# Optimization experiments

Hardware: AMD Instinct MI355X
Metric: run time of the kernel (lower is better)

Reference implementation:

```python
import jax, jax.numpy as jnp
import numpy as np

B = 2          # graphs (images)
GRID = 13      # patches per spatial dim -> N = 169 patches per image
N = GRID * GRID
NN = B * N     # total nodes
C = 256        # hidden_dim / out_channels per head
H = 4          # attention heads
L = 3          # GAT layers
LRELU_SLOPE = 0.2
LN_EPS = 1e-5


def _dense_edges():
    # fully-connected directed graph (i != j) per image, as in create_graph
    idx = np.arange(N)
    src, dst = np.meshgrid(idx, idx, indexing='ij')
    mask = src != dst
    src, dst = src[mask], dst[mask]              # [N*(N-1)]
    offs = (np.arange(B) * N)[:, None]
    e_src = (src[None, :] + offs).reshape(-1)
    e_dst = (dst[None, :] + offs).reshape(-1)
    return e_src.astype(np.int32), e_dst.astype(np.int32)


def setup_inputs() -> dict:
    key = jax.random.key(0)
    ks = jax.random.split(key, 8)
    s = 0.05
    e_src, e_dst = _dense_edges()
    return {
        'x':   jax.random.normal(ks[0], (NN, C), jnp.float32),
        'Wl':  jax.random.normal(ks[1], (L, C, H * C), jnp.float32) * s,
        'bl':  jnp.zeros((L, H * C), jnp.float32),
        'Wr':  jax.random.normal(ks[2], (L, C, H * C), jnp.float32) * s,
        'br':  jnp.zeros((L, H * C), jnp.float32),
        'att': jax.random.normal(ks[3], (L, H, C), jnp.float32) * s,
        'bias': jnp.zeros((L, C), jnp.float32),
        'ln_g': jnp.ones((L, C), jnp.float32),
        'ln_b': jnp.zeros((L, C), jnp.float32),
        'W1':  jax.random.normal(ks[4], (L, C, 2 * C), jnp.float32) * s,
        'b1':  jnp.zeros((L, 2 * C), jnp.float32),
        'W2':  jax.random.normal(ks[5], (L, 2 * C, C), jnp.float32) * s,
        'b2':  jnp.zeros((L, C), jnp.float32),
        'edge_src': jnp.asarray(e_src),
        'edge_dst': jnp.asarray(e_dst),
        'batch_ids': jnp.repeat(jnp.arange(B, dtype=jnp.int32), N),
    }


def _gatv2(x, Wl, bl, Wr, br, att, bias, src, dst, n_nodes):
    # PyG GATv2Conv, concat=False (mean over heads)
    xl = (x @ Wl + bl).reshape(n_nodes, H, C)   # source transform
    xr = (x @ Wr + br).reshape(n_nodes, H, C)   # target transform
    e = jax.nn.leaky_relu(xl[src] + xr[dst], LRELU_SLOPE)     # [E,H,C]
    logits = jnp.einsum('ehc,hc->eh', e, att)                 # [E,H]
    m = jax.ops.segment_max(logits, dst, num_segments=n_nodes)
    a = jnp.exp(logits - m[dst])
    z = jax.ops.segment_sum(a, dst, num_segments=n_nodes)
    alpha = a / (z[dst] + 1e-16)                              # softmax per target
    msg = alpha[:, :, None] * xl[src]                         # [E,H,C]
    agg = jax.ops.segment_sum(msg, dst, num_segments=n_nodes) # [N,H,C]
    return agg.mean(axis=1) + bias


def _layernorm(x, g, b):
    mu = x.mean(-1, keepdims=True)
    var = jnp.mean((x - mu) ** 2, -1, keepdims=True)
    return (x - mu) * jax.lax.rsqrt(var + LN_EPS) * g + b


def reference(x, Wl, bl, Wr, br, att, bias, ln_g, ln_b, W1, b1, W2, b2,
              edge_src, edge_dst, batch_ids):
    n_nodes = x.shape[0]
    for l in range(L):
        residual = x
        h = _gatv2(x, Wl[l], bl[l], Wr[l], br[l], att[l], bias[l],
                   edge_src, edge_dst, n_nodes)
        h = _layernorm(h, ln_g[l], ln_b[l])
        mlp = jnp.maximum(h @ W1[l] + b1[l], 0.0) @ W2[l] + b2[l]
        x = residual + mlp
    # global mean pool per graph
    sums = jax.ops.segment_sum(x, batch_ids, num_segments=B)
    cnts = jax.ops.segment_sum(jnp.ones((n_nodes, 1), x.dtype), batch_ids,
                               num_segments=B)
    return sums / cnts
```

## Files before the change

### kernel.cpp

```cpp
#include <hip/hip_runtime.h>
#include <hip/hip_bf16.h>

typedef __hip_bfloat16 bf16;
typedef __attribute__((ext_vector_type(8))) short short8v;
typedef __attribute__((ext_vector_type(4))) float float4v;

#define NNODES 169
#define NNTOT  338
#define CH     256
#define NH     4
#define NL     3
#define SPAD   176
#define TPAD   177
#define M1PAD  536
#define LN_EPS 1e-5f

__device__ __forceinline__ float b2f(bf16 v) { return __bfloat162float(v); }
__device__ __forceinline__ float lrelu(float v) { return fmaxf(v, 0.2f * v); }
__device__ __forceinline__ float ldm(const void* p, size_t i, int isbf) {
    return isbf ? b2f(((const bf16*)p)[i]) : ((const float*)p)[i];
}
__device__ __forceinline__ short f2bf(float f) {
    union { float f; unsigned u; } x; x.f = f;
    return (short)((x.u + 0x7FFFu + ((x.u >> 16) & 1u)) >> 16);
}
__device__ __forceinline__ int sniff_bf(const void* lng) {
    return ((((const unsigned*)lng)[0] & 0xFFFFu) == 0x3F80u) ? 1 : 0;
}

__global__ __launch_bounds__(256) void k_wt(
    const void* __restrict__ Wl, const void* __restrict__ Wr,
    const void* __restrict__ W1, const void* __restrict__ W2,
    short* __restrict__ wlT, short* __restrict__ wrT,
    short* __restrict__ w1T, short* __restrict__ w2T,
    const void* __restrict__ lng)
{
    __shared__ float s_t[32][33];
    const int isbf = sniff_bf(lng);
    const int z = blockIdx.z, mat = z & 3, l = z >> 2;
    const void* src; short* dst; int K, N;
    if      (mat == 0) { src = Wl; dst = wlT; K = CH;     N = NH * CH; }
    else if (mat == 1) { src = Wr; dst = wrT; K = CH;     N = NH * CH; }
    else if (mat == 2) { src = W1; dst = w1T; K = CH;     N = 2 * CH;  }
    else               { src = W2; dst = w2T; K = 2 * CH; N = CH;      }
    const int tiles = (K >> 5) * (N >> 5);
    if ((int)blockIdx.x >= tiles) return;
    const int tn = blockIdx.x % (N >> 5), tk = blockIdx.x / (N >> 5);
    const int k0 = tk * 32, n0 = tn * 32;
    const size_t lKN = (size_t)l * K * N;
    const int tx = threadIdx.x & 31, ty = threadIdx.x >> 5;

    for (int r = ty; r < 32; r += 8)
        s_t[r][tx] = ldm(src, lKN + (size_t)(k0 + r) * N + n0 + tx, isbf);
    __syncthreads();
    for (int r = ty; r < 32; r += 8)
        dst[lKN + (size_t)(n0 + r) * K + k0 + tx] = f2bf(s_t[tx][r]);
}

template<int KK, int ACT, int RES>
__device__ __forceinline__ void mfma_gemm(
    short* __restrict__ sA, short* __restrict__ sBT,
    const void* __restrict__ Av, int a_bf,
    const short* __restrict__ WT,
    const void* __restrict__ bv_, size_t oB, int isbf,
    const void* __restrict__ x_res, int r_bf,
    float* __restrict__ out,
    int M, int N, int row0, int col0)
{
    const int STR = KK + 8;
    const int tid = threadIdx.x, lane = tid & 63, w = tid >> 6;
    const int r = tid >> 2, q = tid & 3;
    const int kseg = KK / 4, kb0 = q * kseg;
    const int m = lane & 15, kb = (lane >> 4) * 8;
    const int w16 = w * 16;

    {
        const int gr = row0 + r;
        const int ok = (gr < M);
        if (a_bf) {
            const bf16* ap = (const bf16*)Av + (size_t)gr * KK + kb0;
            #pragma unroll
            for (int j = 0; j < kseg; j += 8) {
                int4 v = ok ? *(const int4*)(ap + j) : make_int4(0, 0, 0, 0);
                *(int4*)&sA[r * STR + kb0 + j] = v;
            }
        } else {
            const float* ap = (const float*)Av + (size_t)gr * KK + kb0;
            #pragma unroll
            for (int j = 0; j < kseg; j += 8) {
                short v8[8];
                if (ok) {
                    const float4 f0 = *(const float4*)(ap + j);
                    const float4 f1 = *(const float4*)(ap + j + 4);
                    v8[0] = f2bf(f0.x); v8[1] = f2bf(f0.y);
                    v8[2] = f2bf(f0.z); v8[3] = f2bf(f0.w);
                    v8[4] = f2bf(f1.x); v8[5] = f2bf(f1.y);
                    v8[6] = f2bf(f1.z); v8[7] = f2bf(f1.w);
                } else {
                    #pragma unroll
                    for (int u = 0; u < 8; u++) v8[u] = 0;
                }
                *(int4*)&sA[r * STR + kb0 + j] = *(int4*)v8;
            }
        }
        const short* bp = WT + (size_t)(col0 + r) * KK + kb0;
        #pragma unroll
        for (int j = 0; j < kseg; j += 8)
            *(int4*)&sBT[r * STR + kb0 + j] = *(const int4*)(bp + j);
    }
    __syncthreads();

    float4v acc[4];
    #pragma unroll
    for (int t = 0; t < 4; t++) acc[t] = (float4v){0.f, 0.f, 0.f, 0.f};

    #pragma unroll
    for (int kc = 0; kc < KK / 32; kc++) {
        const short8v af = *(const short8v*)&sA[(w16 + m) * STR + kc * 32 + kb];
        #pragma unroll
        for (int t = 0; t < 4; t++) {
            const short8v bfv = *(const short8v*)&sBT[(t * 16 + m) * STR + kc * 32 + kb];
            acc[t] = __builtin_amdgcn_mfma_f32_16x16x32_bf16(af, bfv, acc[t], 0, 0, 0);
        }
    }

    const int rq = (lane >> 4) * 4;
    #pragma unroll
    for (int t = 0; t < 4; t++) {
        const int col = col0 + t * 16 + m;
        const float bias_v = ldm(bv_, oB + col, isbf);
        #pragma unroll
        for (int rr = 0; rr < 4; rr++) {
            const int gr = row0 + w16 + rq + rr;
            if (gr >= M) continue;
            float v = acc[t][rr] + bias_v;
            if (ACT) v = fmaxf(v, 0.f);
            if (RES) v += ldm(x_res, (size_t)gr * N + col, r_bf);
            out[(size_t)gr * N + col] = v;
        }
    }
}

__global__ __launch_bounds__(256) void k_gemm_lr(
    const void* __restrict__ Av, int israw,
    const short* __restrict__ wlT, const short* __restrict__ wrT, size_t oWT,
    const void* __restrict__ bl, const void* __restrict__ br, size_t oB,
    float* __restrict__ xl, float* __restrict__ xr,
    const void* __restrict__ lng)
{
    __shared__ short sA[64 * 264];
    __shared__ short sBT[64 * 264];
    const int isbf = sniff_bf(lng);
    const int a_bf = israw ? isbf : 0;
    const int row0 = blockIdx.x * 64, col0 = blockIdx.y * 64;
    if (blockIdx.z == 0)
        mfma_gemm<256,0,0>(sA, sBT, Av, a_bf, wlT + oWT, bl, oB, isbf,
                           nullptr, 0, xl, NNTOT, NH * CH, row0, col0);
    else
        mfma_gemm<256,0,0>(sA, sBT, Av, a_bf, wrT + oWT, br, oB, isbf,
                           nullptr, 0, xr, NNTOT, NH * CH, row0, col0);
}

__global__ __launch_bounds__(256) void k_logits_sm(
    const float* __restrict__ xl, const float* __restrict__ xr,
    const void* __restrict__ att, size_t oA,
    float* __restrict__ alphaR, const void* __restrict__ lng)
{
    __shared__ float s_att[CH];
    __shared__ float s_xr[4 * CH];
    __shared__ float s_tile[64 * TPAD];
    __shared__ float s_log[4 * SPAD];
    const int isbf = sniff_bf(lng);
    const int g = blockIdx.z, h = blockIdx.y, d0 = blockIdx.x * 4;
    const int tid = threadIdx.x, lane = tid & 63, wv = tid >> 6;

    s_att[tid] = ldm(att, oA + h * CH + tid, isbf);
    #pragma unroll
    for (int i = 0; i < 4; i++) {
        const int d = d0 + i;
        s_xr[i * CH + tid] = (d < NNODES)
            ? xr[(size_t)(g * NNODES + d) * (NH * CH) + h * CH + tid] : 0.f;
    }

    float l0 = 0.f, l1 = 0.f, l2 = 0.f, l3 = 0.f;
    const int s = tid;
    for (int ch = 0; ch < 4; ch++) {
        __syncthreads();
        for (int i = tid; i < SPAD * 16; i += 256) {
            const int si = i >> 4, c4 = (i & 15) * 4;
            const float4 v = (si < NNODES)
                ? *(const float4*)(xl + (size_t)(g * NNODES + si) * (NH * CH)
                                   + h * CH + ch * 64 + c4)
                : make_float4(0.f, 0.f, 0.f, 0.f);
            s_tile[(c4 + 0) * TPAD + si] = v.x;
            s_tile[(c4 + 1) * TPAD + si] = v.y;
            s_tile[(c4 + 2) * TPAD + si] = v.z;
            s_tile[(c4 + 3) * TPAD + si] = v.w;
        }
        __syncthreads();
        if (s < NNODES) {
            const int cb = ch * 64;
            #pragma unroll 8
            for (int c = 0; c < 64; c++) {
                const float v = s_tile[c * TPAD + s];
                const float a = s_att[cb + c];
                l0 += a * lrelu(v + s_xr[cb + c]);
                l1 += a * lrelu(v + s_xr[CH + cb + c]);
                l2 += a * lrelu(v + s_xr[2 * CH + cb + c]);
                l3 += a * lrelu(v + s_xr[3 * CH + cb + c]);
            }
        }
    }
    if (s < NNODES) {
        s_log[s] = l0; s_log[SPAD + s] = l1;
        s_log[2 * SPAD + s] = l2; s_log[3 * SPAD + s] = l3;
    }
    __syncthreads();

    {
        const int d = d0 + wv;
        const float* row = s_log + wv * SPAD;
        const int s0 = lane, s1 = lane + 64, s2 = lane + 128;
        const float v0 = (s0 < NNODES && s0 != d) ? row[s0] : -1e30f;
        const float v1 = (s1 < NNODES && s1 != d) ? row[s1] : -1e30f;
        const float v2 = (s2 < NNODES && s2 != d) ? row[s2] : -1e30f;
        float mx = fmaxf(v0, fmaxf(v1, v2));
        mx = fmaxf(mx, __shfl_xor(mx, 32)); mx = fmaxf(mx, __shfl_xor(mx, 16));
        mx = fmaxf(mx, __shfl_xor(mx, 8));  mx = fmaxf(mx, __shfl_xor(mx, 4));
        mx = fmaxf(mx, __shfl_xor(mx, 2));  mx = fmaxf(mx, __shfl_xor(mx, 1));
        const float e0 = expf(v0 - mx), e1 = expf(v1 - mx), e2 = expf(v2 - mx);
        float z = e0 + e1 + e2;
        z += __shfl_xor(z, 32); z += __shfl_xor(z, 16); z += __shfl_xor(z, 8);
        z += __shfl_xor(z, 4);  z += __shfl_xor(z, 2);  z += __shfl_xor(z, 1);
        const float sc = 0.25f / (z + 1e-16f);
        if (d < NNODES) {
            float* arow = alphaR + ((size_t)(g * NH + h) * NNODES + d) * SPAD;
            if (s0 < NNODES) arow[s0] = e0 * sc;
            if (s1 < NNODES) arow[s1] = e1 * sc;
            if (s2 < NNODES) arow[s2] = e2 * sc;
        }
    }
}

__global__ __launch_bounds__(256) void k_agg(
    const float* __restrict__ alphaR, const float* __restrict__ xl,
    float* __restrict__ part)
{
    __shared__ float s_a[32 * 33];
    __shared__ float s_x[32 * 64];
    const int gh = blockIdx.z, g = gh >> 2, h = gh & 3;
    const int d0 = blockIdx.x * 32, c0 = blockIdx.y * 64;
    const int tid = threadIdx.x;
    const int dr = (tid >> 4) * 2, cq = (tid & 15) * 4;
    const int sr = tid >> 3, sc4 = (tid & 7) * 4;
    const int xc8 = (tid & 7) * 8;

    float acc[2][4] = {{0.f,0.f,0.f,0.f},{0.f,0.f,0.f,0.f}};

    for (int s0 = 0; s0 < NNODES; s0 += 32) {
        __syncthreads();
        {
            const int d = d0 + sr;
            const float* ap = alphaR + ((size_t)gh * NNODES + d) * SPAD + s0 + sc4;
            const int ok = (d < NNODES);
            s_a[sr * 33 + sc4 + 0] = (ok && s0 + sc4 + 0 < NNODES) ? ap[0] : 0.f;
            s_a[sr * 33 + sc4 + 1] = (ok && s0 + sc4 + 1 < NNODES) ? ap[1] : 0.f;
            s_a[sr * 33 + sc4 + 2] = (ok && s0 + sc4 + 2 < NNODES) ? ap[2] : 0.f;
            s_a[sr * 33 + sc4 + 3] = (ok && s0 + sc4 + 3 < NNODES) ? ap[3] : 0.f;
        }
        {
            const int sg = s0 + sr;
            if (sg < NNODES) {
                const float* xp = xl + (size_t)(g * NNODES + sg) * (NH * CH) + h * CH + c0 + xc8;
                *(float4*)&s_x[sr * 64 + xc8]     = *(const float4*)(xp);
                *(float4*)&s_x[sr * 64 + xc8 + 4] = *(const float4*)(xp + 4);
            } else {
                #pragma unroll
                for (int j = 0; j < 8; j++) s_x[sr * 64 + xc8 + j] = 0.f;
            }
        }
        __syncthreads();
        #pragma unroll
        for (int k = 0; k < 32; k++) {
            const float a0 = s_a[(dr + 0) * 33 + k];
            const float a1 = s_a[(dr + 1) * 33 + k];
            const float4 xv = *(const float4*)&s_x[k * 64 + cq];
            acc[0][0] += a0 * xv.x; acc[0][1] += a0 * xv.y;
            acc[0][2] += a0 * xv.z; acc[0][3] += a0 * xv.w;
            acc[1][0] += a1 * xv.x; acc[1][1] += a1 * xv.y;
            acc[1][2] += a1 * xv.z; acc[1][3] += a1 * xv.w;
        }
    }
    #pragma unroll
    for (int i = 0; i < 2; i++) {
        const int d = d0 + dr + i;
        if (d >= NNODES) continue;
        float4 v;
        v.x = acc[i][0]; v.y = acc[i][1]; v.z = acc[i][2]; v.w = acc[i][3];
        *(float4*)(part + ((size_t)h * NNTOT + g * NNODES + d) * CH + c0 + cq) = v;
    }
}

__global__ __launch_bounds__(256) void k_ln(
    const float* __restrict__ part,
    const void* __restrict__ bias, size_t oB,
    const void* __restrict__ ln_g, size_t oG,
    const void* __restrict__ ln_b, size_t oBt,
    float* __restrict__ h_out, const void* __restrict__ lng)
{
    __shared__ float s_red[8];
    const int isbf = sniff_bf(lng);
    const int node = blockIdx.x, c = threadIdx.x;
    const int lane = c & 63, wv = c >> 6;

    float vch = part[((size_t)0 * NNTOT + node) * CH + c]
              + part[((size_t)1 * NNTOT + node) * CH + c]
              + part[((size_t)2 * NNTOT + node) * CH + c]
              + part[((size_t)3 * NNTOT + node) * CH + c]
              + ldm(bias, oB + c, isbf);

    float s1 = vch, s2 = vch * vch;
    s1 += __shfl_xor(s1, 32); s2 += __shfl_xor(s2, 32);
    s1 += __shfl_xor(s1, 16); s2 += __shfl_xor(s2, 16);
    s1 += __shfl_xor(s1, 8);  s2 += __shfl_xor(s2, 8);
    s1 += __shfl_xor(s1, 4);  s2 += __shfl_xor(s2, 4);
    s1 += __shfl_xor(s1, 2);  s2 += __shfl_xor(s2, 2);
    s1 += __shfl_xor(s1, 1);  s2 += __shfl_xor(s2, 1);
    if (lane == 0) { s_red[wv] = s1; s_red[4 + wv] = s2; }
    __syncthreads();
    const float S1 = s_red[0] + s_red[1] + s_red[2] + s_red[3];
    const float S2 = s_red[4] + s_red[5] + s_red[6] + s_red[7];
    const float mu  = S1 * (1.f / CH);
    const float var = S2 * (1.f / CH) - mu * mu;
    const float o = (vch - mu) * rsqrtf(var + LN_EPS) * ldm(ln_g, oG + c, isbf)
                  + ldm(ln_b, oBt + c, isbf);
    h_out[(size_t)node * CH + c] = o;
}

__global__ __launch_bounds__(256) void k_mlp(
    const float* __restrict__ h_ln,
    const short* __restrict__ w1T, size_t oW1T,
    const void* __restrict__ b1, size_t oB1,
    const short* __restrict__ w2T, size_t oW2T,
    const void* __restrict__ b2, size_t oB2,
    const void* __restrict__ x_res, int israw,
    float* __restrict__ out, const void* __restrict__ lng)
{
    __shared__ short sA[16 * 264];
    __shared__ short sM1[16 * M1PAD];
    __shared__ short sW[64 * 520];
    const int isbf = sniff_bf(lng);
    const int r_bf = israw ? isbf : 0;
    const int g = blockIdx.y;
    const int d0 = blockIdx.x * 16;
    const int tid = threadIdx.x, lane = tid & 63, w = tid >> 6;
    const int m = lane & 15, kb = (lane >> 4) * 8, rq = (lane >> 4) * 4;
    const int w16 = w * 16;

    for (int i = tid; i < 16 * 64; i += 256) {
        const int si = i >> 6, c4 = (i & 63) * 4;
        const int d = d0 + si;
        const float4 v = (d < NNODES)
            ? *(const float4*)(h_ln + (size_t)(g * NNODES + d) * CH + c4)
            : make_float4(0.f, 0.f, 0.f, 0.f);
        short v4[4] = { f2bf(v.x), f2bf(v.y), f2bf(v.z), f2bf(v.w) };
        *(int2*)&sA[si * 264 + c4] = *(int2*)v4;
    }

    for (int nc = 0; nc < 8; nc++) {
        __syncthreads();
        for (int i = tid; i < 64 * 32; i += 256) {
            const int r = i >> 5, k8 = (i & 31) * 8;
            *(int4*)&sW[r * 264 + k8] =
                *(const int4*)(w1T + oW1T + (size_t)(nc * 64 + r) * 256 + k8);
        }
        __syncthreads();
        float4v acc = {0.f, 0.f, 0.f, 0.f};
        #pragma unroll
        for (int kc = 0; kc < 8; kc++) {
            const short8v af = *(const short8v*)&sA[m * 264 + kc * 32 + kb];
            const short8v bfv = *(const short8v*)&sW[(w16 + m) * 264 + kc * 32 + kb];
            acc = __builtin_amdgcn_mfma_f32_16x16x32_bf16(af, bfv, acc, 0, 0, 0);
        }
        const int ng = nc * 64 + w16 + m;
        const float bv = ldm(b1, oB1 + ng, isbf);
        #pragma unroll
        for (int rr = 0; rr < 4; rr++)
            sM1[(rq + rr) * M1PAD + ng] = f2bf(fmaxf(acc[rr] + bv, 0.f));
    }

    for (int nc = 0; nc < 4; nc++) {
        __syncthreads();
        for (int i = tid; i < 64 * 64; i += 256) {
            const int r = i >> 6, k8 = (i & 63) * 8;
            *(int4*)&sW[r * 520 + k8] =
                *(const int4*)(w2T + oW2T + (size_t)(nc * 64 + r) * 512 + k8);
        }
        __syncthreads();
        float4v acc = {0.f, 0.f, 0.f, 0.f};
        #pragma unroll
        for (int kc = 0; kc < 16; kc++) {
            const short8v af = *(const short8v*)&sM1[m * M1PAD + kc * 32 + kb];
            const short8v bfv = *(const short8v*)&sW[(w16 + m) * 520 + kc * 32 + kb];
            acc = __builtin_amdgcn_mfma_f32_16x16x32_bf16(af, bfv, acc, 0, 0, 0);
        }
        const int ng = nc * 64 + w16 + m;
        const float bv = ldm(b2, oB2 + ng, isbf);
        #pragma unroll
        for (int rr = 0; rr < 4; rr++) {
            const int d = d0 + rq + rr;
            if (d < NNODES) {
                const size_t ro = (size_t)(g * NNODES + d) * CH + ng;
                out[ro] = acc[rr] + bv + ldm(x_res, ro, r_bf);
            }
        }
    }
}

__global__ __launch_bounds__(256) void k_pool(const float* __restrict__ x,
                                              void* __restrict__ out,
                                              const void* __restrict__ lng) {
    const int isbf = sniff_bf(lng);
    const int g = blockIdx.x, c = threadIdx.x;
    float s = 0.f;
    const float* p = x + (size_t)g * NNODES * CH + c;
    #pragma unroll 8
    for (int n = 0; n < NNODES; n++) s += p[(size_t)n * CH];
    const float v = s * (1.f / NNODES);
    if (isbf) ((bf16*)out)[g * CH + c] = __float2bfloat16(v);
    else      ((float*)out)[g * CH + c] = v;
}

extern "C" void kernel_launch(void* const* d_in, const int* in_sizes, int n_in,
                              void* d_out, int out_size, void* d_ws, size_t ws_size,
                              hipStream_t stream)
{
    const void* x_in = d_in[0];
    const void* Wl   = d_in[1];
    const void* bl   = d_in[2];
    const void* Wr   = d_in[3];
    const void* br   = d_in[4];
    const void* att  = d_in[5];
    const void* bias = d_in[6];
    const void* lng  = d_in[7];
    const void* lnb  = d_in[8];
    const void* W1   = d_in[9];
    const void* b1   = d_in[10];
    const void* W2   = d_in[11];
    const void* b2   = d_in[12];

    float* ws     = (float*)d_ws;
    float* xl     = ws;
    float* xr     = xl + (size_t)NNTOT * NH * CH;
    float* alphaR = xr + (size_t)NNTOT * NH * CH;
    float* part   = alphaR + (size_t)2 * NH * NNODES * SPAD;
    float* h_ln   = part + (size_t)NH * NNTOT * CH;
    float* xa     = h_ln + (size_t)NNTOT * CH;
    float* xb     = xa + (size_t)NNTOT * CH;
    short* wlT    = (short*)(xb + (size_t)NNTOT * CH);
    short* wrT    = wlT + (size_t)NL * CH * NH * CH;
    short* w1T    = wrT + (size_t)NL * CH * NH * CH;
    short* w2T    = w1T + (size_t)NL * CH * 2 * CH;

    const size_t sB  = NH * CH;
    const size_t sA  = NH * CH;
    const size_t sC  = CH;
    const size_t sB1 = 2 * CH;
    const size_t sWT  = (size_t)CH * NH * CH;
    const size_t sW1T = (size_t)CH * 2 * CH;
    const size_t sW2T = (size_t)2 * CH * CH;

    k_wt<<<dim3(256, 1, 12), 256, 0, stream>>>(
        Wl, Wr, W1, W2, wlT, wrT, w1T, w2T, lng);

    const void* x_l[3] = { x_in, xa, xb };
    float*      x_o[3] = { xa, xb, xa };

    for (int l = 0; l < NL; l++) {
        const int israw = (l == 0);
        k_gemm_lr<<<dim3(6, 16, 2), 256, 0, stream>>>(
            x_l[l], israw, wlT, wrT, (size_t)l * sWT,
            bl, br, (size_t)l * sB, xl, xr, lng);
        k_logits_sm<<<dim3(43, NH, 2), 256, 0, stream>>>(
            xl, xr, att, (size_t)l * sA, alphaR, lng);
        k_agg<<<dim3(6, 4, 8), 256, 0, stream>>>(alphaR, xl, part);
        k_ln<<<dim3(NNTOT), 256, 0, stream>>>(
            part, bias, (size_t)l * sC, lng, (size_t)l * sC, lnb, (size_t)l * sC,
            h_ln, lng);
        k_mlp<<<dim3(11, 2), 256, 0, stream>>>(
            h_ln, w1T, (size_t)l * sW1T, b1, (size_t)l * sB1,
            w2T, (size_t)l * sW2T, b2, (size_t)l * sC,
            x_l[l], israw, x_o[l], lng);
    }

    k_pool<<<dim3(2), 256, 0, stream>>>(xa, d_out, lng);
}
```

Measured before the change: 395.2 us.

## Fuse LayerNorm into MLP first GEMM, split MLP into tiled kernels, widen logits block

LayerNorm is folded into a new kernel that also runs the first MLP GEMM over 64x64 output tiles on a 6x8 grid. The second MLP GEMM moves to the shared mfma_gemm helper on a 6x4 grid. The old MLP kernel ran on only 22 blocks, so this targets low parallelism and the h_ln round trip. In exchange, each first-GEMM block recomputes LayerNorm for its rows, and the intermediate m1 goes to global memory in fp32. The logits kernel now handles 8 destinations per block instead of 4, halving its grid, which reuses each xl tile more at the cost of more registers.

```diff
diff --git a/kernel.cpp b/kernel.cpp
--- a/kernel.cpp
+++ b/kernel.cpp
@@ -12,7 +12,6 @@
 #define NL     3
 #define SPAD   176
 #define TPAD   177
-#define M1PAD  536
 #define LN_EPS 1e-5f
 
 __device__ __forceinline__ float b2f(bf16 v) { return __bfloat162float(v); }
@@ -167,22 +166,22 @@
     float* __restrict__ alphaR, const void* __restrict__ lng)
 {
     __shared__ float s_att[CH];
-    __shared__ float s_xr[4 * CH];
+    __shared__ float s_xr[8 * CH];
     __shared__ float s_tile[64 * TPAD];
-    __shared__ float s_log[4 * SPAD];
-    const int isbf = sniff_bf(lng);
-    const int g = blockIdx.z, h = blockIdx.y, d0 = blockIdx.x * 4;
+    __shared__ float s_log[8 * SPAD];
+    const int isbf = sniff_bf(lng);
+    const int g = blockIdx.z, h = blockIdx.y, d0 = blockIdx.x * 8;
     const int tid = threadIdx.x, lane = tid & 63, wv = tid >> 6;
 
     s_att[tid] = ldm(att, oA + h * CH + tid, isbf);
     #pragma unroll
-    for (int i = 0; i < 4; i++) {
+    for (int i = 0; i < 8; i++) {
         const int d = d0 + i;
         s_xr[i * CH + tid] = (d < NNODES)
             ? xr[(size_t)(g * NNODES + d) * (NH * CH) + h * CH + tid] : 0.f;
     }
 
-    float l0 = 0.f, l1 = 0.f, l2 = 0.f, l3 = 0.f;
+    float l[8] = {0.f, 0.f, 0.f, 0.f, 0.f, 0.f, 0.f, 0.f};
     const int s = tid;
     for (int ch = 0; ch < 4; ch++) {
         __syncthreads();
@@ -200,26 +199,27 @@
         __syncthreads();
         if (s < NNODES) {
             const int cb = ch * 64;
-            #pragma unroll 8
+            #pragma unroll 4
             for (int c = 0; c < 64; c++) {
                 const float v = s_tile[c * TPAD + s];
                 const float a = s_att[cb + c];
-                l0 += a * lrelu(v + s_xr[cb + c]);
-                l1 += a * lrelu(v + s_xr[CH + cb + c]);
-                l2 += a * lrelu(v + s_xr[2 * CH + cb + c]);
-                l3 += a * lrelu(v + s_xr[3 * CH + cb + c]);
+                #pragma unroll
+                for (int i = 0; i < 8; i++)
+                    l[i] += a * lrelu(v + s_xr[i * CH + cb + c]);
             }
         }
     }
     if (s < NNODES) {
-        s_log[s] = l0; s_log[SPAD + s] = l1;
-        s_log[2 * SPAD + s] = l2; s_log[3 * SPAD + s] = l3;
-    }
-    __syncthreads();
-
-    {
-        const int d = d0 + wv;
-        const float* row = s_log + wv * SPAD;
+        #pragma unroll
+        for (int i = 0; i < 8; i++) s_log[i * SPAD + s] = l[i];
+    }
+    __syncthreads();
+
+    #pragma unroll
+    for (int p = 0; p < 2; p++) {
+        const int ri = p * 4 + wv;
+        const int d = d0 + ri;
+        const float* row = s_log + ri * SPAD;
         const int s0 = lane, s1 = lane + 64, s2 = lane + 128;
         const float v0 = (s0 < NNODES && s0 != d) ? row[s0] : -1e30f;
         const float v1 = (s1 < NNODES && s1 != d) ? row[s1] : -1e30f;
@@ -301,120 +301,120 @@
     }
 }
 
-__global__ __launch_bounds__(256) void k_ln(
+__global__ __launch_bounds__(256) void k_lnmlp1(
     const float* __restrict__ part,
     const void* __restrict__ bias, size_t oB,
     const void* __restrict__ ln_g, size_t oG,
     const void* __restrict__ ln_b, size_t oBt,
-    float* __restrict__ h_out, const void* __restrict__ lng)
-{
-    __shared__ float s_red[8];
-    const int isbf = sniff_bf(lng);
-    const int node = blockIdx.x, c = threadIdx.x;
-    const int lane = c & 63, wv = c >> 6;
-
-    float vch = part[((size_t)0 * NNTOT + node) * CH + c]
-              + part[((size_t)1 * NNTOT + node) * CH + c]
-              + part[((size_t)2 * NNTOT + node) * CH + c]
-              + part[((size_t)3 * NNTOT + node) * CH + c]
-              + ldm(bias, oB + c, isbf);
-
-    float s1 = vch, s2 = vch * vch;
-    s1 += __shfl_xor(s1, 32); s2 += __shfl_xor(s2, 32);
-    s1 += __shfl_xor(s1, 16); s2 += __shfl_xor(s2, 16);
-    s1 += __shfl_xor(s1, 8);  s2 += __shfl_xor(s2, 8);
-    s1 += __shfl_xor(s1, 4);  s2 += __shfl_xor(s2, 4);
-    s1 += __shfl_xor(s1, 2);  s2 += __shfl_xor(s2, 2);
-    s1 += __shfl_xor(s1, 1);  s2 += __shfl_xor(s2, 1);
-    if (lane == 0) { s_red[wv] = s1; s_red[4 + wv] = s2; }
-    __syncthreads();
-    const float S1 = s_red[0] + s_red[1] + s_red[2] + s_red[3];
-    const float S2 = s_red[4] + s_red[5] + s_red[6] + s_red[7];
-    const float mu  = S1 * (1.f / CH);
-    const float var = S2 * (1.f / CH) - mu * mu;
-    const float o = (vch - mu) * rsqrtf(var + LN_EPS) * ldm(ln_g, oG + c, isbf)
-                  + ldm(ln_b, oBt + c, isbf);
-    h_out[(size_t)node * CH + c] = o;
-}
-
-__global__ __launch_bounds__(256) void k_mlp(
-    const float* __restrict__ h_ln,
     const short* __restrict__ w1T, size_t oW1T,
     const void* __restrict__ b1, size_t oB1,
-    const short* __restrict__ w2T, size_t oW2T,
-    const void* __restrict__ b2, size_t oB2,
-    const void* __restrict__ x_res, int israw,
-    float* __restrict__ out, const void* __restrict__ lng)
-{
-    __shared__ short sA[16 * 264];
-    __shared__ short sM1[16 * M1PAD];
-    __shared__ short sW[64 * 520];
-    const int isbf = sniff_bf(lng);
-    const int r_bf = israw ? isbf : 0;
-    const int g = blockIdx.y;
-    const int d0 = blockIdx.x * 16;
+    float* __restrict__ m1, const void* __restrict__ lng)
+{
+    __shared__ float s_row[64 * 260];
+    __shared__ short sA[64 * 264];
+    __shared__ short sW[64 * 264];
+    __shared__ float s_red[64 * 8];
+    const int isbf = sniff_bf(lng);
+    const int row0 = blockIdx.x * 64, col0 = blockIdx.y * 64;
     const int tid = threadIdx.x, lane = tid & 63, w = tid >> 6;
     const int m = lane & 15, kb = (lane >> 4) * 8, rq = (lane >> 4) * 4;
     const int w16 = w * 16;
-
-    for (int i = tid; i < 16 * 64; i += 256) {
-        const int si = i >> 6, c4 = (i & 63) * 4;
-        const int d = d0 + si;
-        const float4 v = (d < NNODES)
-            ? *(const float4*)(h_ln + (size_t)(g * NNODES + d) * CH + c4)
-            : make_float4(0.f, 0.f, 0.f, 0.f);
-        short v4[4] = { f2bf(v.x), f2bf(v.y), f2bf(v.z), f2bf(v.w) };
-        *(int2*)&sA[si * 264 + c4] = *(int2*)v4;
-    }
-
-    for (int nc = 0; nc < 8; nc++) {
-        __syncthreads();
-        for (int i = tid; i < 64 * 32; i += 256) {
-            const int r = i >> 5, k8 = (i & 31) * 8;
-            *(int4*)&sW[r * 264 + k8] =
-                *(const int4*)(w1T + oW1T + (size_t)(nc * 64 + r) * 256 + k8);
-        }
-        __syncthreads();
-        float4v acc = {0.f, 0.f, 0.f, 0.f};
-        #pragma unroll
-        for (int kc = 0; kc < 8; kc++) {
-            const short8v af = *(const short8v*)&sA[m * 264 + kc * 32 + kb];
-            const short8v bfv = *(const short8v*)&sW[(w16 + m) * 264 + kc * 32 + kb];
-            acc = __builtin_amdgcn_mfma_f32_16x16x32_bf16(af, bfv, acc, 0, 0, 0);
-        }
-        const int ng = nc * 64 + w16 + m;
-        const float bv = ldm(b1, oB1 + ng, isbf);
-        #pragma unroll
-        for (int rr = 0; rr < 4; rr++)
-            sM1[(rq + rr) * M1PAD + ng] = f2bf(fmaxf(acc[rr] + bv, 0.f));
-    }
-
-    for (int nc = 0; nc < 4; nc++) {
-        __syncthreads();
-        for (int i = tid; i < 64 * 64; i += 256) {
-            const int r = i >> 6, k8 = (i & 63) * 8;
-            *(int4*)&sW[r * 520 + k8] =
-                *(const int4*)(w2T + oW2T + (size_t)(nc * 64 + r) * 512 + k8);
-        }
-        __syncthreads();
-        float4v acc = {0.f, 0.f, 0.f, 0.f};
-        #pragma unroll
-        for (int kc = 0; kc < 16; kc++) {
-            const short8v af = *(const short8v*)&sM1[m * M1PAD + kc * 32 + kb];
-            const short8v bfv = *(const short8v*)&sW[(w16 + m) * 520 + kc * 32 + kb];
-            acc = __builtin_amdgcn_mfma_f32_16x16x32_bf16(af, bfv, acc, 0, 0, 0);
-        }
-        const int ng = nc * 64 + w16 + m;
-        const float bv = ldm(b2, oB2 + ng, isbf);
+    const int r = tid >> 2, q = tid & 3, cb = q * 64;
+
+    for (int i = tid; i < 64 * 32; i += 256) {
+        const int rr = i >> 5, k8 = (i & 31) * 8;
+        *(int4*)&sW[rr * 264 + k8] =
+            *(const int4*)(w1T + oW1T + (size_t)(col0 + rr) * 256 + k8);
+    }
+
+    {
+        const int gr = row0 + r;
+        float s1 = 0.f, s2 = 0.f;
+        if (gr < NNTOT) {
+            for (int c = cb; c < cb + 64; c += 4) {
+                const float4 v0 = *(const float4*)(part + ((size_t)0 * NNTOT + gr) * CH + c);
+                const float4 v1 = *(const float4*)(part + ((size_t)1 * NNTOT + gr) * CH + c);
+                const float4 v2 = *(const float4*)(part + ((size_t)2 * NNTOT + gr) * CH + c);
+                const float4 v3 = *(const float4*)(part + ((size_t)3 * NNTOT + gr) * CH + c);
+                float4 o;
+                o.x = v0.x + v1.x + v2.x + v3.x + ldm(bias, oB + c + 0, isbf);
+                o.y = v0.y + v1.y + v2.y + v3.y + ldm(bias, oB + c + 1, isbf);
+                o.z = v0.z + v1.z + v2.z + v3.z + ldm(bias, oB + c + 2, isbf);
+                o.w = v0.w + v1.w + v2.w + v3.w + ldm(bias, oB + c + 3, isbf);
+                *(float4*)&s_row[r * 260 + c] = o;
+                s1 += o.x + o.y + o.z + o.w;
+                s2 += o.x * o.x + o.y * o.y + o.z * o.z + o.w * o.w;
+            }
+        } else {
+            for (int c = cb; c < cb + 64; c += 4)
+                *(float4*)&s_row[r * 260 + c] = make_float4(0.f, 0.f, 0.f, 0.f);
+        }
+        s_red[r * 8 + q * 2 + 0] = s1;
+        s_red[r * 8 + q * 2 + 1] = s2;
+    }
+    __syncthreads();
+    if (tid < 64) {
+        const float S1 = s_red[tid * 8 + 0] + s_red[tid * 8 + 2]
+                       + s_red[tid * 8 + 4] + s_red[tid * 8 + 6];
+        const float S2 = s_red[tid * 8 + 1] + s_red[tid * 8 + 3]
+                       + s_red[tid * 8 + 5] + s_red[tid * 8 + 7];
+        const float mu  = S1 * (1.f / CH);
+        const float var = S2 * (1.f / CH) - mu * mu;
+        s_red[tid * 8 + 0] = mu;
+        s_red[tid * 8 + 1] = rsqrtf(var + LN_EPS);
+    }
+    __syncthreads();
+    {
+        const float mu = s_red[r * 8 + 0], rs = s_red[r * 8 + 1];
+        for (int c = cb; c < cb + 64; c += 4) {
+            const float4 v = *(const float4*)&s_row[r * 260 + c];
+            short v4[4];
+            v4[0] = f2bf((v.x - mu) * rs * ldm(ln_g, oG + c + 0, isbf) + ldm(ln_b, oBt + c + 0, isbf));
+            v4[1] = f2bf((v.y - mu) * rs * ldm(ln_g, oG + c + 1, isbf) + ldm(ln_b, oBt + c + 1, isbf));
+            v4[2] = f2bf((v.z - mu) * rs * ldm(ln_g, oG + c + 2, isbf) + ldm(ln_b, oBt + c + 2, isbf));
+            v4[3] = f2bf((v.w - mu) * rs * ldm(ln_g, oG + c + 3, isbf) + ldm(ln_b, oBt + c + 3, isbf));
+            *(int2*)&sA[r * 264 + c] = *(int2*)v4;
+        }
+    }
+    __syncthreads();
+
+    float4v acc[4];
+    #pragma unroll
+    for (int t = 0; t < 4; t++) acc[t] = (float4v){0.f, 0.f, 0.f, 0.f};
+    #pragma unroll
+    for (int kc = 0; kc < 8; kc++) {
+        const short8v af = *(const short8v*)&sA[(w16 + m) * 264 + kc * 32 + kb];
+        #pragma unroll
+        for (int t = 0; t < 4; t++) {
+            const short8v bfv = *(const short8v*)&sW[(t * 16 + m) * 264 + kc * 32 + kb];
+            acc[t] = __builtin_amdgcn_mfma_f32_16x16x32_bf16(af, bfv, acc[t], 0, 0, 0);
+        }
+    }
+    #pragma unroll
+    for (int t = 0; t < 4; t++) {
+        const int col = col0 + t * 16 + m;
+        const float bv = ldm(b1, oB1 + col, isbf);
         #pragma unroll
         for (int rr = 0; rr < 4; rr++) {
-            const int d = d0 + rq + rr;
-            if (d < NNODES) {
-                const size_t ro = (size_t)(g * NNODES + d) * CH + ng;
-                out[ro] = acc[rr] + bv + ldm(x_res, ro, r_bf);
-            }
-        }
-    }
+            const int gr = row0 + w16 + rq + rr;
+            if (gr >= NNTOT) continue;
+            m1[(size_t)gr * (2 * CH) + col] = fmaxf(acc[t][rr] + bv, 0.f);
+        }
+    }
+}
+
+__global__ __launch_bounds__(256) void k_mlp2(
+    const float* __restrict__ A, const short* __restrict__ w2T, size_t oWT,
+    const void* __restrict__ b, size_t oB,
+    const void* __restrict__ x_res, int israw,
+    float* __restrict__ out, const void* __restrict__ lng)
+{
+    __shared__ short sA[64 * 520];
+    __shared__ short sBT[64 * 520];
+    const int isbf = sniff_bf(lng);
+    const int r_bf = israw ? isbf : 0;
+    mfma_gemm<512,0,1>(sA, sBT, A, 0, w2T + oWT, b, oB, isbf, x_res, r_bf,
+                       out, NNTOT, CH, blockIdx.x * 64, blockIdx.y * 64);
 }
 
 __global__ __launch_bounds__(256) void k_pool(const float* __restrict__ x,
@@ -454,8 +454,8 @@
     float* xr     = xl + (size_t)NNTOT * NH * CH;
     float* alphaR = xr + (size_t)NNTOT * NH * CH;
     float* part   = alphaR + (size_t)2 * NH * NNODES * SPAD;
-    float* h_ln   = part + (size_t)NH * NNTOT * CH;
-    float* xa     = h_ln + (size_t)NNTOT * CH;
+    float* m1     = part + (size_t)NH * NNTOT * CH;
+    float* xa     = m1 + (size_t)NNTOT * 2 * CH;
     float* xb     = xa + (size_t)NNTOT * CH;
     short* wlT    = (short*)(xb + (size_t)NNTOT * CH);
     short* wrT    = wlT + (size_t)NL * CH * NH * CH;
@@ -463,7 +463,7 @@
     short* w2T    = w1T + (size_t)NL * CH * 2 * CH;
 
     const size_t sB  = NH * CH;
-    const size_t sA  = NH * CH;
+    const size_t sA_ = NH * CH;
     const size_t sC  = CH;
     const size_t sB1 = 2 * CH;
     const size_t sWT  = (size_t)CH * NH * CH;
@@ -481,15 +481,14 @@
         k_gemm_lr<<<dim3(6, 16, 2), 256, 0, stream>>>(
             x_l[l], israw, wlT, wrT, (size_t)l * sWT,
             bl, br, (size_t)l * sB, xl, xr, lng);
-        k_logits_sm<<<dim3(43, NH, 2), 256, 0, stream>>>(
-            xl, xr, att, (size_t)l * sA, alphaR, lng);
+        k_logits_sm<<<dim3(22, NH, 2), 256, 0, stream>>>(
+            xl, xr, att, (size_t)l * sA_, alphaR, lng);
         k_agg<<<dim3(6, 4, 8), 256, 0, stream>>>(alphaR, xl, part);
-        k_ln<<<dim3(NNTOT), 256, 0, stream>>>(
+        k_lnmlp1<<<dim3(6, 8), 256, 0, stream>>>(
             part, bias, (size_t)l * sC, lng, (size_t)l * sC, lnb, (size_t)l * sC,
-            h_ln, lng);
-        k_mlp<<<dim3(11, 2), 256, 0, stream>>>(
-            h_ln, w1T, (size_t)l * sW1T, b1, (size_t)l * sB1,
-            w2T, (size_t)l * sW2T, b2, (size_t)l * sC,
+            w1T, (size_t)l * sW1T, b1, (size_t)l * sB1, m1, lng);
+        k_mlp2<<<dim3(6, 4), 256, 0, stream>>>(
+            m1, w2T, (size_t)l * sW2T, b2, (size_t)l * sC,
             x_l[l], israw, x_o[l], lng);
     }
 
```

After: 388.7 us. Within noise of the previous version (-1.7%).
